# Kernel tuning notes

Measured on AMD Instinct MI355X. Metric: run time of the kernel, lower is better.

## Reference

```python
import jax, jax.numpy as jnp
import numpy as np

N, S, D, d, H = 8, 2048, 256, 128, 10  # H = rel_k_heights
SCALING = float(np.sqrt(2 * d))


def _ln(x, g, b):
    m = jnp.mean(x, axis=-1, keepdims=True)
    v = jnp.var(x, axis=-1, keepdims=True)
    return (x - m) / jnp.sqrt(v + 1e-5) * g + b


def setup_inputs() -> dict:
    key = jax.random.key(0)
    ks = jax.random.split(key, 12)
    std = 0.02
    p = lambda k, shape: (jax.random.normal(k, shape, jnp.float32) * std)
    return {
        'sequence': jax.random.normal(ks[0], (N, S, D), jnp.float32),
        'attention_mask': jax.random.bernoulli(ks[1], 0.9, (N, S, S)),
        'heights': jax.random.randint(ks[2], (N, S), 0, 50),
        'W_init': p(ks[3], (D, D)), 'b_init': jnp.zeros((D,), jnp.float32),
        'ln_g': jnp.ones((D,), jnp.float32), 'ln_b': jnp.zeros((D,), jnp.float32),
        'W_U': p(ks[4], (D, 2 * D)), 'b_U': jnp.zeros((2 * D,), jnp.float32),
        'W_V': p(ks[5], (D, 2 * D)), 'b_V': jnp.zeros((2 * D,), jnp.float32),
        'W_Z': p(ks[6], (D, d)), 'b_Z': jnp.zeros((d,), jnp.float32),
        'os_gamma': p(ks[7], (3, d)),  # torch inits gamma ~ N(0, 0.02)
        'os_beta': jnp.zeros((3, d), jnp.float32),
        'embed_heights': jax.random.normal(ks[8], (H, d), jnp.float32),
        'W_out': p(ks[9], (2 * D, D)), 'b_out': jnp.zeros((D,), jnp.float32),
        'W_gate': p(ks[10], (2 * D, D)), 'b_gate': jnp.zeros((D,), jnp.float32),
    }


def reference(sequence, attention_mask, heights,
              W_init, b_init, ln_g, ln_b,
              W_U, b_U, W_V, b_V, W_Z, b_Z,
              os_gamma, os_beta, embed_heights,
              W_out, b_out, W_gate, b_gate):
    S0 = (S - 1) // 2  # 1023
    mask = attention_mask[:, :S0, S0:]          # [N,S0,S1]
    res = sequence

    x = _ln(sequence @ W_init + b_init, ln_g, ln_b)            # [N,S,D]
    U = jax.nn.silu(x[:, :S0, :] @ W_U + b_U)                  # [N,S0,2D]
    Z = jax.nn.silu(x @ W_Z + b_Z)                             # [N,S,d]
    V = jax.nn.silu(x[:, S0:, :] @ W_V + b_V)                  # [N,S1,2D]

    # OffsetScale: Q, Qp, K from Z
    Q = (Z * os_gamma[0] + os_beta[0])[:, :S0, :]              # [N,S0,d]
    Qp = (Z * os_gamma[1] + os_beta[1])[:, :S0, :]             # [N,S0,d]
    K = (Z * os_gamma[2] + os_beta[2])[:, S0:, :]              # [N,S1,d]

    energy = jnp.einsum('bsd,btd->bst', Q, K)                  # [N,S0,S1]

    # relative-height bias: direct gather (math-equivalent to one-hot*sum)
    Q_h = jnp.einsum('bsd,hd->bsh', Qp, embed_heights)         # [N,S0,H]
    rel = heights[:, None, S0:] - heights[:, :S0, None]        # [N,S0,S1]
    rel_idx = jnp.clip(rel, 1, H) - 1
    rel_energy = jnp.take_along_axis(Q_h, rel_idx, axis=2)     # [N,S0,S1]

    logits = (energy + rel_energy) / SCALING
    logits = jnp.where(mask, logits, -9999.0)
    attn = jax.nn.softmax(logits, axis=-1)                     # [N,S0,S1]

    V_ = jnp.einsum('bst,btd->bsd', attn, V)                   # [N,S0,2D]
    out = (U * V_) @ W_out + b_out                             # [N,S0,D]
    gates = jax.nn.sigmoid(
        jnp.concatenate([out, res[:, :S0, :]], axis=-1) @ W_gate + b_gate)
    out = gates * out + (1.0 - gates) * res[:, :S0, :]
    out = jnp.concatenate([out, res[:, S0:, :]], axis=1)       # [N,S,D]
    return out
```

## Files before the change

### kernel.cpp

```cpp
#include <hip/hip_runtime.h>
#include <cstdint>
#include <cstddef>

#define S_TOT 2048
#define S0_   1023
#define S1_   1025
#define D_    256
#define D2_   512
#define DZ_   128
#define NB_   8
#define NT_   17
#define KT16_ 68
#define SCALE_INV (1.0f/16.0f)
#define XPAD  264
#define UPAD  520

typedef __attribute__((ext_vector_type(8))) short short8v;
typedef __attribute__((ext_vector_type(4))) short short4v;
typedef __attribute__((ext_vector_type(4))) float f32x4;
typedef unsigned long long u64;

__device__ __forceinline__ short f2bf(float f){
  unsigned u = __float_as_uint(f);
  unsigned r = (u + 0x7FFFu + ((u >> 16) & 1u)) >> 16;
  return (short)r;
}
__device__ __forceinline__ float bf2f(short s){
  return __uint_as_float(((unsigned)(unsigned short)s) << 16);
}
__device__ __forceinline__ float silu_f(float x){ return x / (1.f + __expf(-x)); }

__device__ __forceinline__ short8v load_afrag(const short* arow, int kt, int khi){
  short4v lo = *reinterpret_cast<const short4v*>(arow + kt*32 + khi);
  short4v hi = *reinterpret_cast<const short4v*>(arow + kt*32 + khi + 16);
  short8v r = {lo[0],lo[1],lo[2],lo[3],hi[0],hi[1],hi[2],hi[3]};
  return r;
}

__global__ __launch_bounds__(256) void k_prep(
    const float* __restrict__ W_init, const float* __restrict__ W_U,
    const float* __restrict__ W_V,    const float* __restrict__ W_Z,
    const float* __restrict__ W_out,  const float* __restrict__ W_gate,
    short* __restrict__ WpI, short* __restrict__ WpU, short* __restrict__ WpV,
    short* __restrict__ WpZ, short* __restrict__ WpO, short* __restrict__ WpG,
    const unsigned char* __restrict__ amask, u64* __restrict__ maskb)
{
  const int blk = blockIdx.x;
  if (blk < 304){
    const float* W; short* dst; int K, N, base;
    if      (blk <  32){ W=W_init; dst=WpI; K=256; N=256; base=0;   }
    else if (blk <  96){ W=W_U;    dst=WpU; K=256; N=512; base=32;  }
    else if (blk < 160){ W=W_V;    dst=WpV; K=256; N=512; base=96;  }
    else if (blk < 176){ W=W_Z;    dst=WpZ; K=256; N=128; base=160; }
    else if (blk < 240){ W=W_out;  dst=WpO; K=512; N=256; base=176; }
    else               { W=W_gate; dst=WpG; K=512; N=256; base=240; }
    const int wv = threadIdx.x >> 6, lane = threadIdx.x & 63;
    const int KT = K >> 5;
    const int tile = (blk - base)*4 + wv;
    const int nt = tile / KT, kt = tile - nt*KT;
    const int n = nt*16 + (lane & 15);
    const int kbase = kt*32 + ((lane>>4)<<2);
    short8v v;
    #pragma unroll
    for (int j=0;j<8;++j){
      int k = kbase + (j&3) + ((j>>2)<<4);
      v[j] = f2bf(W[(size_t)k*N + n]);
    }
    *reinterpret_cast<short8v*>(dst + ((size_t)tile*64 + lane)*8) = v;
  } else {
    const int lane = threadIdx.x & 63;
    const int w = (blk - 304)*4 + (threadIdx.x >> 6);
    if (w >= NB_*S0_*NT_) return;
    int b = w / (S0_*NT_);
    int rem = w - b*(S0_*NT_);
    int q = rem / NT_;
    int t = rem - q*NT_;
    int key = t*64 + lane;
    unsigned char v = 0;
    if (key < S1_) v = amask[((size_t)(b*S_TOT + q))*S_TOT + S0_ + key];
    u64 bits = __ballot(v != 0);
    if (lane == 0) maskb[w] = bits;
  }
}

__global__ __launch_bounds__(256) void k_x(
    const float* __restrict__ seq, const short* __restrict__ Wp,
    const float* __restrict__ b_init,
    const float* __restrict__ ln_g, const float* __restrict__ ln_b,
    short* __restrict__ xb, float* __restrict__ out)
{
  __shared__ short s_a[64*XPAD];
  const int tid = threadIdx.x, lane = tid & 63, wv = tid >> 6;
  const int R0 = blockIdx.x * 64;
  const int colb = lane & 15, khi = (lane>>4)<<2;

  for (int c = tid; c < 64*64; c += 256){
    int row = c >> 6, c4 = (c & 63) << 2;
    int g = R0 + row;
    float4 f = *reinterpret_cast<const float4*>(seq + (size_t)g*D_ + c4);
    short4v h = { f2bf(f.x), f2bf(f.y), f2bf(f.z), f2bf(f.w) };
    *reinterpret_cast<short4v*>(&s_a[row*XPAD + c4]) = h;
    if ((g & 2047) >= S0_)
      *reinterpret_cast<float4*>(out + (size_t)g*D_ + c4) = f;
  }
  __syncthreads();

  f32x4 acc[16];
  #pragma unroll
  for (int nt=0;nt<16;++nt) acc[nt] = (f32x4){0.f,0.f,0.f,0.f};

  const short* arow = &s_a[(wv*16 + colb)*XPAD];
  #pragma unroll
  for (int kt=0; kt<8; ++kt){
    short8v a = load_afrag(arow, kt, khi);
    #pragma unroll
    for (int nt=0; nt<16; ++nt){
      short8v b = *reinterpret_cast<const short8v*>(Wp + ((size_t)(nt*8 + kt)*64 + lane)*8);
      acc[nt] = __builtin_amdgcn_mfma_f32_16x16x32_bf16(a, b, acc[nt], 0, 0, 0);
    }
  }

  float sum[4] = {0.f,0.f,0.f,0.f};
  #pragma unroll
  for (int nt=0; nt<16; ++nt){
    float bv = b_init[nt*16 + colb];
    #pragma unroll
    for (int r=0;r<4;++r){ acc[nt][r] += bv; sum[r] += acc[nt][r]; }
  }
  #pragma unroll
  for (int r=0;r<4;++r){
    #pragma unroll
    for (int m=1;m<16;m<<=1) sum[r] += __shfl_xor(sum[r], m, 64);
    sum[r] *= (1.f/256.f);
  }
  float var[4] = {0.f,0.f,0.f,0.f};
  #pragma unroll
  for (int nt=0; nt<16; ++nt)
    #pragma unroll
    for (int r=0;r<4;++r){ float d = acc[nt][r]-sum[r]; var[r] += d*d; }
  #pragma unroll
  for (int r=0;r<4;++r){
    #pragma unroll
    for (int m=1;m<16;m<<=1) var[r] += __shfl_xor(var[r], m, 64);
    var[r] = rsqrtf(var[r]*(1.f/256.f) + 1e-5f);
  }
  #pragma unroll
  for (int nt=0; nt<16; ++nt){
    int col = nt*16 + colb;
    float g = ln_g[col], bb = ln_b[col];
    #pragma unroll
    for (int r=0;r<4;++r){
      float xn = (acc[nt][r]-sum[r])*var[r]*g + bb;
      s_a[(wv*16 + ((lane>>4)<<2) + r)*XPAD + col] = f2bf(xn);
    }
  }
  __syncthreads();
  for (int c = tid; c < 64*32; c += 256){
    int row = c >> 5, c8 = (c & 31) << 3;
    *reinterpret_cast<short8v*>(xb + (size_t)(R0+row)*D_ + c8) =
        *reinterpret_cast<const short8v*>(&s_a[row*XPAD + c8]);
  }
}

__global__ __launch_bounds__(256) void k_gemmZ(
    const short* __restrict__ xb, const short* __restrict__ Wp,
    const float* __restrict__ bias, short* __restrict__ Zb)
{
  __shared__ short s_a[64*XPAD];
  const int tid = threadIdx.x, lane = tid & 63, wv = tid >> 6;
  const int wy = wv >> 1, wx = wv & 1;
  const int R0 = blockIdx.x * 64;
  const int C0 = blockIdx.y * 64;
  const int colb = lane & 15, khi = (lane>>4)<<2;

  for (int c = tid; c < 64*32; c += 256){
    int r = c >> 5, c8 = (c & 31) << 3;
    size_t xrow = (size_t)(R0 + r);
    *reinterpret_cast<short8v*>(&s_a[r*XPAD + c8]) =
        *reinterpret_cast<const short8v*>(xb + xrow*D_ + c8);
  }
  __syncthreads();

  f32x4 acc[2][2];
  #pragma unroll
  for(int i=0;i<2;++i)
    #pragma unroll
    for(int j=0;j<2;++j) acc[i][j] = (f32x4){0.f,0.f,0.f,0.f};

  const short* ar0 = &s_a[(wy*32 + colb)*XPAD];
  const short* ar1 = ar0 + 16*XPAD;
  const int ntg = (C0 >> 4) + wx*2;
  #pragma unroll
  for (int kt=0; kt<8; ++kt){
    short8v a0 = load_afrag(ar0, kt, khi);
    short8v a1 = load_afrag(ar1, kt, khi);
    short8v b0 = *reinterpret_cast<const short8v*>(Wp + ((size_t)((ntg+0)*8 + kt)*64 + lane)*8);
    short8v b1 = *reinterpret_cast<const short8v*>(Wp + ((size_t)((ntg+1)*8 + kt)*64 + lane)*8);
    acc[0][0] = __builtin_amdgcn_mfma_f32_16x16x32_bf16(a0, b0, acc[0][0], 0,0,0);
    acc[0][1] = __builtin_amdgcn_mfma_f32_16x16x32_bf16(a0, b1, acc[0][1], 0,0,0);
    acc[1][0] = __builtin_amdgcn_mfma_f32_16x16x32_bf16(a1, b0, acc[1][0], 0,0,0);
    acc[1][1] = __builtin_amdgcn_mfma_f32_16x16x32_bf16(a1, b1, acc[1][1], 0,0,0);
  }
  #pragma unroll
  for (int sj=0; sj<2; ++sj){
    int col = C0 + wx*32 + sj*16 + colb;
    float bv = bias[col];
    #pragma unroll
    for (int si=0; si<2; ++si){
      #pragma unroll
      for (int r=0;r<4;++r){
        int orow = R0 + wy*32 + si*16 + ((lane>>4)<<2) + r;
        Zb[(size_t)orow*DZ_ + col] = f2bf(silu_f(acc[si][sj][r] + bv));
      }
    }
  }
}

__global__ __launch_bounds__(256) void k_packZ(const short* __restrict__ Zb,
                                               short* __restrict__ ZkF){
  const int lane = threadIdx.x & 63;
  const int w = blockIdx.x*4 + (threadIdx.x >> 6);
  if (w >= NB_*KT16_*4) return;
  const int b = w / (KT16_*4);
  const int rem = w - b*(KT16_*4);
  const int kt16 = rem >> 2, kt = rem & 3;
  int key = kt16*16 + (lane & 15); if (key > 1024) key = 1024;
  const short* zr = Zb + ((size_t)(b*S_TOT + S0_ + key))*DZ_ + kt*32 + ((lane>>4)<<2);
  short4v lo = *reinterpret_cast<const short4v*>(zr);
  short4v hi = *reinterpret_cast<const short4v*>(zr + 16);
  short8v f = {lo[0],lo[1],lo[2],lo[3],hi[0],hi[1],hi[2],hi[3]};
  *reinterpret_cast<short8v*>(ZkF + ((size_t)w*64 + lane)*8) = f;
}

__global__ __launch_bounds__(256) void k_gemmV(
    const short* __restrict__ xb, const short* __restrict__ Wp,
    const float* __restrict__ bias, short* __restrict__ VtF)
{
  __shared__ short s_a[64*XPAD];
  __shared__ short s_t[64][72];
  const int tid = threadIdx.x, lane = tid & 63, wv = tid >> 6;
  const int wy = wv >> 1, wx = wv & 1;
  const int R0 = blockIdx.x * 64;
  const int C0 = blockIdx.y * 64;
  const int b  = blockIdx.z;
  const int colb = lane & 15, khi = (lane>>4)<<2;

  for (int c = tid; c < 64*32; c += 256){
    int r = c >> 5, c8 = (c & 31) << 3;
    int k = R0 + r; if (k > 1024) k = 1024;
    size_t xrow = (size_t)b*S_TOT + S0_ + k;
    *reinterpret_cast<short8v*>(&s_a[r*XPAD + c8]) =
        *reinterpret_cast<const short8v*>(xb + xrow*D_ + c8);
  }
  __syncthreads();

  f32x4 acc[2][2];
  #pragma unroll
  for(int i=0;i<2;++i)
    #pragma unroll
    for(int j=0;j<2;++j) acc[i][j] = (f32x4){0.f,0.f,0.f,0.f};

  const short* ar0 = &s_a[(wy*32 + colb)*XPAD];
  const short* ar1 = ar0 + 16*XPAD;
  const int ntg = (C0 >> 4) + wx*2;
  #pragma unroll
  for (int kt=0; kt<8; ++kt){
    short8v a0 = load_afrag(ar0, kt, khi);
    short8v a1 = load_afrag(ar1, kt, khi);
    short8v b0 = *reinterpret_cast<const short8v*>(Wp + ((size_t)((ntg+0)*8 + kt)*64 + lane)*8);
    short8v b1 = *reinterpret_cast<const short8v*>(Wp + ((size_t)((ntg+1)*8 + kt)*64 + lane)*8);
    acc[0][0] = __builtin_amdgcn_mfma_f32_16x16x32_bf16(a0, b0, acc[0][0], 0,0,0);
    acc[0][1] = __builtin_amdgcn_mfma_f32_16x16x32_bf16(a0, b1, acc[0][1], 0,0,0);
    acc[1][0] = __builtin_amdgcn_mfma_f32_16x16x32_bf16(a1, b0, acc[1][0], 0,0,0);
    acc[1][1] = __builtin_amdgcn_mfma_f32_16x16x32_bf16(a1, b1, acc[1][1], 0,0,0);
  }
  #pragma unroll
  for (int sj=0; sj<2; ++sj){
    int cl = wx*32 + sj*16 + colb;
    float bv = bias[C0 + cl];
    #pragma unroll
    for (int si=0; si<2; ++si){
      #pragma unroll
      for (int r=0;r<4;++r){
        int rl = wy*32 + si*16 + ((lane>>4)<<2) + r;
        s_t[cl][rl] = f2bf(silu_f(acc[si][sj][r] + bv));
      }
    }
  }
  __syncthreads();
  {
    const int vt_l = tid >> 6;
    const int vloc = vt_l*16 + (lane & 15);
    const int krow = (lane>>4)<<2;
    const int t = R0 >> 6;
    #pragma unroll
    for (int kt=0; kt<2; ++kt){
      short8v f;
      #pragma unroll
      for (int j=0;j<8;++j){
        int kl = kt*32 + krow + (j&3) + ((j>>2)<<4);
        short v = s_t[vloc][kl];
        if (R0 + kl >= S1_) v = 0;
        f[j] = v;
      }
      size_t o = (((size_t)b*32 + (C0>>4) + vt_l)*(2*NT_) + 2*t + kt)*64 + lane;
      *reinterpret_cast<short8v*>(VtF + o*8) = f;
    }
  }
}

#define SMEM_BYTES 51712
__global__ __launch_bounds__(256,2) void k_flash(
    const short* __restrict__ Zb, const short* __restrict__ ZkF,
    const short* __restrict__ VtF, const u64* __restrict__ maskb,
    const short* __restrict__ xb,
    const short* __restrict__ WpU, const float* __restrict__ b_U,
    const short* __restrict__ Wpo, const float* __restrict__ b_out,
    const short* __restrict__ Wpg, const float* __restrict__ b_gate,
    const float* __restrict__ seq, float* __restrict__ out,
    const int* __restrict__ heights,
    const float* __restrict__ os_g, const float* __restrict__ os_b,
    const float* __restrict__ embH)
{
  __shared__ __align__(16) char smem[SMEM_BYTES];
  __shared__ float  s_qh[16][12];
  __shared__ float  s_qb[16];
  __shared__ int    s_hk[NT_*64];
  __shared__ u64    s_mb[16][NT_];
  __shared__ float  s_mx[4][16];
  __shared__ float  s_sm[4][16];

  short8v (*s_pl)[64] = reinterpret_cast<short8v(*)[64]>(smem);
  short8v (*s_ph)[64] = reinterpret_cast<short8v(*)[64]>(smem + 17408);
  short   (*s_qg)[132] = reinterpret_cast<short(*)[132]>(smem);
  short* sUV = reinterpret_cast<short*>(smem);
  short* sO  = reinterpret_cast<short*>(smem + 16640);
  short* sX  = reinterpret_cast<short*>(smem + 34816);
  short* sR  = reinterpret_cast<short*>(smem + 43264);

  const int tid = threadIdx.x, lane = tid & 63, wv = tid >> 6;
  const int b  = blockIdx.x & 7;
  const int qt = blockIdx.x >> 3;
  const int q0 = qt * 16;

  for (int c = tid; c < 16*32; c += 256){
    int r = c >> 5, c8 = (c & 31) << 3;
    int q = min(q0 + r, S0_-1);
    *reinterpret_cast<short8v*>(&sX[r*XPAD + c8]) =
        *reinterpret_cast<const short8v*>(xb + ((size_t)(b*S_TOT + q))*D_ + c8);
  }
  for (int c = tid; c < 16*64; c += 256){
    int r = c >> 6, c4 = (c & 63) << 2;
    int q = min(q0 + r, S0_-1);
    float4 f = *reinterpret_cast<const float4*>(seq + ((size_t)(b*S_TOT + q))*D_ + c4);
    short4v h = { f2bf(f.x), f2bf(f.y), f2bf(f.z), f2bf(f.w) };
    *reinterpret_cast<short4v*>(&sR[r*XPAD + c4]) = h;
  }

  {
    int row = tid >> 4, part = tid & 15;
    int q = q0 + row; if (q > S0_-1) q = S0_-1;
    const short* zrow = Zb + ((size_t)(b*S_TOT + q))*DZ_ + part*8;
    float qb_acc = 0.f;
    float qh_acc[10];
    #pragma unroll
    for (int h=0;h<10;++h) qh_acc[h] = 0.f;
    #pragma unroll
    for (int e=0; e<8; ++e){
      int dz = part*8 + e;
      float z = bf2f(zrow[e]);
      float Q  = z*os_g[dz]      + os_b[dz];
      float Qp = z*os_g[DZ_+dz]  + os_b[DZ_+dz];
      s_qg[row][dz] = f2bf(Q * os_g[2*DZ_+dz]);
      qb_acc += Q * os_b[2*DZ_+dz];
      #pragma unroll
      for (int h=0;h<10;++h) qh_acc[h] += Qp * embH[h*DZ_ + dz];
    }
    #pragma unroll
    for (int m=1;m<16;m<<=1){
      qb_acc += __shfl_xor(qb_acc, m, 64);
      #pragma unroll
      for (int h=0;h<10;++h) qh_acc[h] += __shfl_xor(qh_acc[h], m, 64);
    }
    if (part == 0){
      s_qb[row] = qb_acc;
      #pragma unroll
      for (int h=0;h<10;++h) s_qh[row][h] = qh_acc[h];
    }
  }
  for (int k = tid; k < NT_*64; k += 256)
    s_hk[k] = (k < S1_) ? heights[b*S_TOT + S0_ + k] : 0;
  for (int idx = tid; idx < 16*NT_; idx += 256){
    int qq = idx / NT_, tt = idx - qq*NT_;
    int qr = q0 + qq; if (qr > S0_-1) qr = S0_-1;
    s_mb[qq][tt] = maskb[((size_t)(b*S0_ + qr))*NT_ + tt];
  }
  __syncthreads();

  const int qcol = lane & 15, khi = (lane>>4)<<2;
  int qme = q0 + qcol; if (qme > S0_-1) qme = S0_-1;
  const int hq = heights[b*S_TOT + qme];
  const float qb = s_qb[qcol];

  short8v qgf[4];
  #pragma unroll
  for (int kt=0; kt<4; ++kt) qgf[kt] = load_afrag(&s_qg[qcol][0], kt, khi);

  f32x4 sc[5][4];
  float tmw = -1e30f;
  #pragma unroll
  for (int it=0; it<5; ++it){
    const int t = it*4 + wv;
    if (t < NT_){
      u64 mb = s_mb[qcol][t];
      #pragma unroll
      for (int st=0; st<4; ++st){
        f32x4 c = (f32x4){0.f,0.f,0.f,0.f};
        #pragma unroll
        for (int kt=0; kt<4; ++kt){
          short8v a = *reinterpret_cast<const short8v*>(
              ZkF + (((size_t)(b*KT16_ + t*4 + st)*4 + kt)*64 + lane)*8);
          c = __builtin_amdgcn_mfma_f32_16x16x32_bf16(a, qgf[kt], c, 0,0,0);
        }
        int4 hk4 = *reinterpret_cast<const int4*>(&s_hk[t*64 + st*16 + khi]);
        #pragma unroll
        for (int r=0;r<4;++r){
          int hk = (&hk4.x)[r];
          int idx = min(max(hk - hq, 1), 10) - 1;
          float v = (c[r] + qb + s_qh[qcol][idx]) * SCALE_INV;
          int kl = st*16 + khi + r;
          v = ((mb >> kl) & 1ull) ? v : -9999.f;
          c[r] = v;
          tmw = fmaxf(tmw, v);
        }
        sc[it][st] = c;
      }
    }
  }
  tmw = fmaxf(tmw, __shfl_xor(tmw, 16, 64));
  tmw = fmaxf(tmw, __shfl_xor(tmw, 32, 64));
  if (lane < 16) s_mx[wv][lane] = tmw;
  __syncthreads();

  const float m = fmaxf(fmaxf(s_mx[0][qcol], s_mx[1][qcol]),
                        fmaxf(s_mx[2][qcol], s_mx[3][qcol]));
  float ls = 0.f;
  #pragma unroll
  for (int it=0; it<5; ++it){
    const int t = it*4 + wv;
    if (t < NT_){
      #pragma unroll
      for (int st=0; st<4; ++st)
        #pragma unroll
        for (int r=0;r<4;++r){
          float p = __expf(sc[it][st][r] - m);
          ls += p;
          sc[it][st][r] = p;
        }
      short8v pa0, pa1;
      #pragma unroll
      for (int j=0;j<8;++j){
        pa0[j] = f2bf(sc[it][(j>>2)][j&3]);
        pa1[j] = f2bf(sc[it][2 + (j>>2)][j&3]);
      }
      s_pl[t][lane] = pa0;
      s_ph[t][lane] = pa1;
    }
  }
  ls += __shfl_xor(ls, 16, 64);
  ls += __shfl_xor(ls, 32, 64);
  if (lane < 16) s_sm[wv][lane] = ls;
  __syncthreads();

  float lrow[4];
  #pragma unroll
  for (int r=0;r<4;++r){
    int qr = khi + r;
    lrow[r] = s_sm[0][qr] + s_sm[1][qr] + s_sm[2][qr] + s_sm[3][qr];
  }
  f32x4 O[8];
  #pragma unroll
  for (int vt=0; vt<8; ++vt) O[vt] = (f32x4){0.f,0.f,0.f,0.f};
  for (int t=0; t<NT_; ++t){
    short8v pa0 = s_pl[t][lane];
    short8v pa1 = s_ph[t][lane];
    #pragma unroll
    for (int vt=0; vt<8; ++vt){
      size_t vb = ((size_t)b*32 + wv*8 + vt)*(2*NT_) + 2*t;
      short8v b0 = *reinterpret_cast<const short8v*>(VtF + (vb*64 + lane)*8);
      short8v b1 = *reinterpret_cast<const short8v*>(VtF + ((vb+1)*64 + lane)*8);
      O[vt] = __builtin_amdgcn_mfma_f32_16x16x32_bf16(pa0, b0, O[vt], 0,0,0);
      O[vt] = __builtin_amdgcn_mfma_f32_16x16x32_bf16(pa1, b1, O[vt], 0,0,0);
    }
  }
  __syncthreads();

  f32x4 accu[8];
  #pragma unroll
  for (int vt=0; vt<8; ++vt) accu[vt] = (f32x4){0.f,0.f,0.f,0.f};
  {
    const short* xrow = &sX[qcol*XPAD];
    #pragma unroll
    for (int kt=0; kt<8; ++kt){
      short8v a = load_afrag(xrow, kt, khi);
      #pragma unroll
      for (int vt=0; vt<8; ++vt){
        int nt = wv*8 + vt;
        short8v bw = *reinterpret_cast<const short8v*>(WpU + ((size_t)(nt*8 + kt)*64 + lane)*8);
        accu[vt] = __builtin_amdgcn_mfma_f32_16x16x32_bf16(a, bw, accu[vt], 0,0,0);
      }
    }
  }
  float inv[4];
  #pragma unroll
  for (int r=0;r<4;++r) inv[r] = 1.f / lrow[r];
  #pragma unroll
  for (int vt=0; vt<8; ++vt){
    int v = wv*128 + vt*16 + qcol;
    float bu = b_U[v];
    #pragma unroll
    for (int r=0;r<4;++r){
      float u = silu_f(accu[vt][r] + bu);
      sUV[(khi + r)*UPAD + v] = f2bf(u * O[vt][r] * inv[r]);
    }
  }
  __syncthreads();

  f32x4 acc_o[4];
  #pragma unroll
  for (int j=0;j<4;++j) acc_o[j] = (f32x4){0.f,0.f,0.f,0.f};
  {
    const short* arow = &sUV[qcol*UPAD];
    #pragma unroll
    for (int kt=0; kt<16; ++kt){
      short8v a = load_afrag(arow, kt, khi);
      #pragma unroll
      for (int j=0;j<4;++j){
        int nt = wv*4 + j;
        short8v bw = *reinterpret_cast<const short8v*>(Wpo + ((size_t)(nt*16 + kt)*64 + lane)*8);
        acc_o[j] = __builtin_amdgcn_mfma_f32_16x16x32_bf16(a, bw, acc_o[j], 0,0,0);
      }
    }
  }
  #pragma unroll
  for (int j=0;j<4;++j){
    int col = (wv*4+j)*16 + qcol;
    float bv = b_out[col];
    #pragma unroll
    for (int r=0;r<4;++r){
      acc_o[j][r] += bv;
      sO[(khi + r)*XPAD + col] = f2bf(acc_o[j][r]);
    }
  }
  __syncthreads();

  f32x4 acc_g[4];
  #pragma unroll
  for (int j=0;j<4;++j) acc_g[j] = (f32x4){0.f,0.f,0.f,0.f};
  {
    const short* orow_p = &sO[qcol*XPAD];
    const short* rrow_p = &sR[qcol*XPAD];
    #pragma unroll
    for (int kt=0; kt<8; ++kt){
      short8v a = load_afrag(orow_p, kt, khi);
      #pragma unroll
      for (int j=0;j<4;++j){
        int nt = wv*4 + j;
        short8v bw = *reinterpret_cast<const short8v*>(Wpg + ((size_t)(nt*16 + kt)*64 + lane)*8);
        acc_g[j] = __builtin_amdgcn_mfma_f32_16x16x32_bf16(a, bw, acc_g[j], 0,0,0);
      }
    }
    #pragma unroll
    for (int kt=0; kt<8; ++kt){
      short8v a = load_afrag(rrow_p, kt, khi);
      #pragma unroll
      for (int j=0;j<4;++j){
        int nt = wv*4 + j;
        short8v bw = *reinterpret_cast<const short8v*>(Wpg + ((size_t)(nt*16 + 8 + kt)*64 + lane)*8);
        acc_g[j] = __builtin_amdgcn_mfma_f32_16x16x32_bf16(a, bw, acc_g[j], 0,0,0);
      }
    }
  }
  #pragma unroll
  for (int j=0;j<4;++j){
    int col = (wv*4+j)*16 + qcol;
    float bg = b_gate[col];
    #pragma unroll
    for (int r=0;r<4;++r){
      int q = q0 + khi + r;
      if (q < S0_){
        float res = seq[((size_t)(b*S_TOT + q))*D_ + col];
        float g = 1.f/(1.f + __expf(-(acc_g[j][r] + bg)));
        out[((size_t)(b*S_TOT + q))*D_ + col] = g*acc_o[j][r] + (1.f-g)*res;
      }
    }
  }
}

extern "C" void kernel_launch(void* const* d_in, const int* in_sizes, int n_in,
                              void* d_out, int out_size, void* d_ws, size_t ws_size,
                              hipStream_t stream)
{
  const float* seq    = (const float*)d_in[0];
  const unsigned char* amask = (const unsigned char*)d_in[1];
  const int*   heights= (const int*)d_in[2];
  const float* W_init = (const float*)d_in[3];
  const float* b_init = (const float*)d_in[4];
  const float* ln_g   = (const float*)d_in[5];
  const float* ln_b   = (const float*)d_in[6];
  const float* W_U    = (const float*)d_in[7];
  const float* b_U    = (const float*)d_in[8];
  const float* W_V    = (const float*)d_in[9];
  const float* b_V    = (const float*)d_in[10];
  const float* W_Z    = (const float*)d_in[11];
  const float* b_Z    = (const float*)d_in[12];
  const float* os_g   = (const float*)d_in[13];
  const float* os_b   = (const float*)d_in[14];
  const float* embH   = (const float*)d_in[15];
  const float* W_out  = (const float*)d_in[16];
  const float* b_out  = (const float*)d_in[17];
  const float* W_gate = (const float*)d_in[18];
  const float* b_gate = (const float*)d_in[19];
  float* out = (float*)d_out;

  char* w = (char*)d_ws;
  short* Zb  = (short*)w;                w += (size_t)16512*128*2;
  short* VtF = (short*)w;                w += (size_t)8*32*(2*NT_)*64*8*2;
  short* ZkF = (short*)w;                w += (size_t)NB_*KT16_*4*64*8*2;
  short* xb  = (short*)w;                w += (size_t)16384*256*2;
  u64*  maskb = (u64*)w;                 w += (size_t)NB_*S0_*NT_*8;
  short* WpI = (short*)w;                w += (size_t)65536*2;
  short* WpU = (short*)w;                w += (size_t)131072*2;
  short* WpV = (short*)w;                w += (size_t)131072*2;
  short* WpZ = (short*)w;                w += (size_t)32768*2;
  short* WpO = (short*)w;                w += (size_t)131072*2;
  short* WpG = (short*)w;                w += (size_t)131072*2;

  hipLaunchKernelGGL(k_prep, dim3(304 + (NB_*S0_*NT_ + 3)/4), dim3(256), 0, stream,
      W_init, W_U, W_V, W_Z, W_out, W_gate,
      WpI, WpU, WpV, WpZ, WpO, WpG, amask, maskb);

  hipLaunchKernelGGL(k_x, dim3(256), dim3(256), 0, stream,
      seq, WpI, b_init, ln_g, ln_b, xb, out);

  hipLaunchKernelGGL(k_gemmZ, dim3(256, 2), dim3(256), 0, stream,
      xb, WpZ, b_Z, Zb);
  hipLaunchKernelGGL(k_packZ, dim3((NB_*KT16_*4 + 3)/4), dim3(256), 0, stream, Zb, ZkF);
  hipLaunchKernelGGL(k_gemmV, dim3(17, 8, 8), dim3(256), 0, stream,
      xb, WpV, b_V, VtF);

  hipLaunchKernelGGL(k_flash, dim3(512), dim3(256), 0, stream,
      Zb, ZkF, VtF, maskb, xb, WpU, b_U, WpO, b_out, WpG, b_gate,
      seq, out, heights, os_g, os_b, embH);
}
```

Measured before the change: 115.6 us.

## Fuse Z GEMM into LN kernel, merge V/packZ/Q-prep into one launch

```diff
diff --git a/kernel.cpp b/kernel.cpp
--- a/kernel.cpp
+++ b/kernel.cpp
@@ -14,6 +14,7 @@
 #define SCALE_INV (1.0f/16.0f)
 #define XPAD  264
 #define UPAD  520
+#define ZPAD  136
 
 typedef __attribute__((ext_vector_type(8))) short short8v;
 typedef __attribute__((ext_vector_type(4))) short short4v;
@@ -87,9 +88,11 @@
     const float* __restrict__ seq, const short* __restrict__ Wp,
     const float* __restrict__ b_init,
     const float* __restrict__ ln_g, const float* __restrict__ ln_b,
-    short* __restrict__ xb, float* __restrict__ out)
+    const short* __restrict__ WpZ, const float* __restrict__ b_Z,
+    short* __restrict__ xb, short* __restrict__ Zb, float* __restrict__ out)
 {
   __shared__ short s_a[64*XPAD];
+  __shared__ short s_z[64*ZPAD];
   const int tid = threadIdx.x, lane = tid & 63, wv = tid >> 6;
   const int R0 = blockIdx.x * 64;
   const int colb = lane & 15, khi = (lane>>4)<<2;
@@ -155,172 +158,184 @@
     }
   }
   __syncthreads();
+
   for (int c = tid; c < 64*32; c += 256){
     int row = c >> 5, c8 = (c & 31) << 3;
     *reinterpret_cast<short8v*>(xb + (size_t)(R0+row)*D_ + c8) =
         *reinterpret_cast<const short8v*>(&s_a[row*XPAD + c8]);
   }
-}
-
-__global__ __launch_bounds__(256) void k_gemmZ(
-    const short* __restrict__ xb, const short* __restrict__ Wp,
-    const float* __restrict__ bias, short* __restrict__ Zb)
-{
-  __shared__ short s_a[64*XPAD];
-  const int tid = threadIdx.x, lane = tid & 63, wv = tid >> 6;
-  const int wy = wv >> 1, wx = wv & 1;
-  const int R0 = blockIdx.x * 64;
-  const int C0 = blockIdx.y * 64;
-  const int colb = lane & 15, khi = (lane>>4)<<2;
-
-  for (int c = tid; c < 64*32; c += 256){
-    int r = c >> 5, c8 = (c & 31) << 3;
-    size_t xrow = (size_t)(R0 + r);
-    *reinterpret_cast<short8v*>(&s_a[r*XPAD + c8]) =
-        *reinterpret_cast<const short8v*>(xb + xrow*D_ + c8);
-  }
-  __syncthreads();
-
-  f32x4 acc[2][2];
-  #pragma unroll
-  for(int i=0;i<2;++i)
-    #pragma unroll
-    for(int j=0;j<2;++j) acc[i][j] = (f32x4){0.f,0.f,0.f,0.f};
-
-  const short* ar0 = &s_a[(wy*32 + colb)*XPAD];
-  const short* ar1 = ar0 + 16*XPAD;
-  const int ntg = (C0 >> 4) + wx*2;
+
+  f32x4 accz[8];
+  #pragma unroll
+  for (int nt=0;nt<8;++nt) accz[nt] = (f32x4){0.f,0.f,0.f,0.f};
   #pragma unroll
   for (int kt=0; kt<8; ++kt){
-    short8v a0 = load_afrag(ar0, kt, khi);
-    short8v a1 = load_afrag(ar1, kt, khi);
-    short8v b0 = *reinterpret_cast<const short8v*>(Wp + ((size_t)((ntg+0)*8 + kt)*64 + lane)*8);
-    short8v b1 = *reinterpret_cast<const short8v*>(Wp + ((size_t)((ntg+1)*8 + kt)*64 + lane)*8);
-    acc[0][0] = __builtin_amdgcn_mfma_f32_16x16x32_bf16(a0, b0, acc[0][0], 0,0,0);
-    acc[0][1] = __builtin_amdgcn_mfma_f32_16x16x32_bf16(a0, b1, acc[0][1], 0,0,0);
-    acc[1][0] = __builtin_amdgcn_mfma_f32_16x16x32_bf16(a1, b0, acc[1][0], 0,0,0);
-    acc[1][1] = __builtin_amdgcn_mfma_f32_16x16x32_bf16(a1, b1, acc[1][1], 0,0,0);
-  }
-  #pragma unroll
-  for (int sj=0; sj<2; ++sj){
-    int col = C0 + wx*32 + sj*16 + colb;
-    float bv = bias[col];
-    #pragma unroll
-    for (int si=0; si<2; ++si){
-      #pragma unroll
-      for (int r=0;r<4;++r){
-        int orow = R0 + wy*32 + si*16 + ((lane>>4)<<2) + r;
-        Zb[(size_t)orow*DZ_ + col] = f2bf(silu_f(acc[si][sj][r] + bv));
-      }
-    }
-  }
-}
-
-__global__ __launch_bounds__(256) void k_packZ(const short* __restrict__ Zb,
-                                               short* __restrict__ ZkF){
-  const int lane = threadIdx.x & 63;
-  const int w = blockIdx.x*4 + (threadIdx.x >> 6);
-  if (w >= NB_*KT16_*4) return;
-  const int b = w / (KT16_*4);
-  const int rem = w - b*(KT16_*4);
-  const int kt16 = rem >> 2, kt = rem & 3;
-  int key = kt16*16 + (lane & 15); if (key > 1024) key = 1024;
-  const short* zr = Zb + ((size_t)(b*S_TOT + S0_ + key))*DZ_ + kt*32 + ((lane>>4)<<2);
-  short4v lo = *reinterpret_cast<const short4v*>(zr);
-  short4v hi = *reinterpret_cast<const short4v*>(zr + 16);
-  short8v f = {lo[0],lo[1],lo[2],lo[3],hi[0],hi[1],hi[2],hi[3]};
-  *reinterpret_cast<short8v*>(ZkF + ((size_t)w*64 + lane)*8) = f;
-}
-
-__global__ __launch_bounds__(256) void k_gemmV(
-    const short* __restrict__ xb, const short* __restrict__ Wp,
-    const float* __restrict__ bias, short* __restrict__ VtF)
+    short8v a = load_afrag(arow, kt, khi);
+    #pragma unroll
+    for (int nt=0; nt<8; ++nt){
+      short8v b = *reinterpret_cast<const short8v*>(WpZ + ((size_t)(nt*8 + kt)*64 + lane)*8);
+      accz[nt] = __builtin_amdgcn_mfma_f32_16x16x32_bf16(a, b, accz[nt], 0,0,0);
+    }
+  }
+  #pragma unroll
+  for (int nt=0; nt<8; ++nt){
+    int col = nt*16 + colb;
+    float bz = b_Z[col];
+    #pragma unroll
+    for (int r=0;r<4;++r)
+      s_z[(wv*16 + khi + r)*ZPAD + col] = f2bf(silu_f(accz[nt][r] + bz));
+  }
+  __syncthreads();
+  for (int c = tid; c < 64*16; c += 256){
+    int row = c >> 4, c8 = (c & 15) << 3;
+    *reinterpret_cast<short8v*>(Zb + (size_t)(R0+row)*DZ_ + c8) =
+        *reinterpret_cast<const short8v*>(&s_z[row*ZPAD + c8]);
+  }
+}
+
+__global__ __launch_bounds__(256) void k_mid(
+    const short* __restrict__ xb, const short* __restrict__ WpV,
+    const float* __restrict__ b_V, short* __restrict__ VtF,
+    const short* __restrict__ Zb, short* __restrict__ ZkF,
+    const float* __restrict__ os_g, const float* __restrict__ os_b,
+    const float* __restrict__ embH,
+    short* __restrict__ Qgb, float* __restrict__ qhb)
 {
   __shared__ short s_a[64*XPAD];
   __shared__ short s_t[64][72];
+  const int blk = blockIdx.x;
   const int tid = threadIdx.x, lane = tid & 63, wv = tid >> 6;
-  const int wy = wv >> 1, wx = wv & 1;
-  const int R0 = blockIdx.x * 64;
-  const int C0 = blockIdx.y * 64;
-  const int b  = blockIdx.z;
-  const int colb = lane & 15, khi = (lane>>4)<<2;
-
-  for (int c = tid; c < 64*32; c += 256){
-    int r = c >> 5, c8 = (c & 31) << 3;
-    int k = R0 + r; if (k > 1024) k = 1024;
-    size_t xrow = (size_t)b*S_TOT + S0_ + k;
-    *reinterpret_cast<short8v*>(&s_a[r*XPAD + c8]) =
-        *reinterpret_cast<const short8v*>(xb + xrow*D_ + c8);
-  }
-  __syncthreads();
-
-  f32x4 acc[2][2];
-  #pragma unroll
-  for(int i=0;i<2;++i)
-    #pragma unroll
-    for(int j=0;j<2;++j) acc[i][j] = (f32x4){0.f,0.f,0.f,0.f};
-
-  const short* ar0 = &s_a[(wy*32 + colb)*XPAD];
-  const short* ar1 = ar0 + 16*XPAD;
-  const int ntg = (C0 >> 4) + wx*2;
-  #pragma unroll
-  for (int kt=0; kt<8; ++kt){
-    short8v a0 = load_afrag(ar0, kt, khi);
-    short8v a1 = load_afrag(ar1, kt, khi);
-    short8v b0 = *reinterpret_cast<const short8v*>(Wp + ((size_t)((ntg+0)*8 + kt)*64 + lane)*8);
-    short8v b1 = *reinterpret_cast<const short8v*>(Wp + ((size_t)((ntg+1)*8 + kt)*64 + lane)*8);
-    acc[0][0] = __builtin_amdgcn_mfma_f32_16x16x32_bf16(a0, b0, acc[0][0], 0,0,0);
-    acc[0][1] = __builtin_amdgcn_mfma_f32_16x16x32_bf16(a0, b1, acc[0][1], 0,0,0);
-    acc[1][0] = __builtin_amdgcn_mfma_f32_16x16x32_bf16(a1, b0, acc[1][0], 0,0,0);
-    acc[1][1] = __builtin_amdgcn_mfma_f32_16x16x32_bf16(a1, b1, acc[1][1], 0,0,0);
-  }
-  #pragma unroll
-  for (int sj=0; sj<2; ++sj){
-    int cl = wx*32 + sj*16 + colb;
-    float bv = bias[C0 + cl];
-    #pragma unroll
-    for (int si=0; si<2; ++si){
-      #pragma unroll
-      for (int r=0;r<4;++r){
-        int rl = wy*32 + si*16 + ((lane>>4)<<2) + r;
-        s_t[cl][rl] = f2bf(silu_f(acc[si][sj][r] + bv));
-      }
-    }
-  }
-  __syncthreads();
-  {
-    const int vt_l = tid >> 6;
-    const int vloc = vt_l*16 + (lane & 15);
-    const int krow = (lane>>4)<<2;
-    const int t = R0 >> 6;
-    #pragma unroll
-    for (int kt=0; kt<2; ++kt){
-      short8v f;
-      #pragma unroll
-      for (int j=0;j<8;++j){
-        int kl = kt*32 + krow + (j&3) + ((j>>2)<<4);
-        short v = s_t[vloc][kl];
-        if (R0 + kl >= S1_) v = 0;
-        f[j] = v;
-      }
-      size_t o = (((size_t)b*32 + (C0>>4) + vt_l)*(2*NT_) + 2*t + kt)*64 + lane;
-      *reinterpret_cast<short8v*>(VtF + o*8) = f;
+
+  if (blk < 1088){
+    const int t   = blk % 17;
+    const int rest= blk / 17;
+    const int C0  = (rest & 7) * 64;
+    const int b   = rest >> 3;
+    const int R0  = t * 64;
+    const int wy = wv >> 1, wx = wv & 1;
+    const int colb = lane & 15, khi = (lane>>4)<<2;
+
+    for (int c = tid; c < 64*32; c += 256){
+      int r = c >> 5, c8 = (c & 31) << 3;
+      int k = R0 + r; if (k > 1024) k = 1024;
+      size_t xrow = (size_t)b*S_TOT + S0_ + k;
+      *reinterpret_cast<short8v*>(&s_a[r*XPAD + c8]) =
+          *reinterpret_cast<const short8v*>(xb + xrow*D_ + c8);
+    }
+    __syncthreads();
+
+    f32x4 acc[2][2];
+    #pragma unroll
+    for(int i=0;i<2;++i)
+      #pragma unroll
+      for(int j=0;j<2;++j) acc[i][j] = (f32x4){0.f,0.f,0.f,0.f};
+
+    const short* ar0 = &s_a[(wy*32 + colb)*XPAD];
+    const short* ar1 = ar0 + 16*XPAD;
+    const int ntg = (C0 >> 4) + wx*2;
+    #pragma unroll
+    for (int kt=0; kt<8; ++kt){
+      short8v a0 = load_afrag(ar0, kt, khi);
+      short8v a1 = load_afrag(ar1, kt, khi);
+      short8v b0 = *reinterpret_cast<const short8v*>(WpV + ((size_t)((ntg+0)*8 + kt)*64 + lane)*8);
+      short8v b1 = *reinterpret_cast<const short8v*>(WpV + ((size_t)((ntg+1)*8 + kt)*64 + lane)*8);
+      acc[0][0] = __builtin_amdgcn_mfma_f32_16x16x32_bf16(a0, b0, acc[0][0], 0,0,0);
+      acc[0][1] = __builtin_amdgcn_mfma_f32_16x16x32_bf16(a0, b1, acc[0][1], 0,0,0);
+      acc[1][0] = __builtin_amdgcn_mfma_f32_16x16x32_bf16(a1, b0, acc[1][0], 0,0,0);
+      acc[1][1] = __builtin_amdgcn_mfma_f32_16x16x32_bf16(a1, b1, acc[1][1], 0,0,0);
+    }
+    #pragma unroll
+    for (int sj=0; sj<2; ++sj){
+      int cl = wx*32 + sj*16 + colb;
+      float bv = b_V[C0 + cl];
+      #pragma unroll
+      for (int si=0; si<2; ++si){
+        #pragma unroll
+        for (int r=0;r<4;++r){
+          int rl = wy*32 + si*16 + ((lane>>4)<<2) + r;
+          s_t[cl][rl] = f2bf(silu_f(acc[si][sj][r] + bv));
+        }
+      }
+    }
+    __syncthreads();
+    {
+      const int vt_l = tid >> 6;
+      const int vloc = vt_l*16 + (lane & 15);
+      const int krow = (lane>>4)<<2;
+      #pragma unroll
+      for (int kt=0; kt<2; ++kt){
+        short8v f;
+        #pragma unroll
+        for (int j=0;j<8;++j){
+          int kl = kt*32 + krow + (j&3) + ((j>>2)<<4);
+          short v = s_t[vloc][kl];
+          if (R0 + kl >= S1_) v = 0;
+          f[j] = v;
+        }
+        size_t o = (((size_t)b*32 + (C0>>4) + vt_l)*(2*NT_) + 2*t + kt)*64 + lane;
+        *reinterpret_cast<short8v*>(VtF + o*8) = f;
+      }
+    }
+  } else if (blk < 1632){
+    const int w = (blk - 1088)*4 + wv;
+    if (w >= NB_*KT16_*4) return;
+    const int b = w / (KT16_*4);
+    const int rem = w - b*(KT16_*4);
+    const int kt16 = rem >> 2, kt = rem & 3;
+    int key = kt16*16 + (lane & 15); if (key > 1024) key = 1024;
+    const short* zr = Zb + ((size_t)(b*S_TOT + S0_ + key))*DZ_ + kt*32 + ((lane>>4)<<2);
+    short4v lo = *reinterpret_cast<const short4v*>(zr);
+    short4v hi = *reinterpret_cast<const short4v*>(zr + 16);
+    short8v f = {lo[0],lo[1],lo[2],lo[3],hi[0],hi[1],hi[2],hi[3]};
+    *reinterpret_cast<short8v*>(ZkF + ((size_t)w*64 + lane)*8) = f;
+  } else {
+    const int idx = blk - 1632;
+    const int b = idx & 7, q0 = (idx >> 3) * 16;
+    int row = tid >> 4, part = tid & 15;
+    int q = q0 + row; if (q > S0_-1) q = S0_-1;
+    const short* zrow = Zb + ((size_t)(b*S_TOT + q))*DZ_ + part*8;
+    float qb_acc = 0.f;
+    float qh_acc[10];
+    #pragma unroll
+    for (int h=0;h<10;++h) qh_acc[h] = 0.f;
+    short8v qgv;
+    #pragma unroll
+    for (int e=0; e<8; ++e){
+      int dz = part*8 + e;
+      float z = bf2f(zrow[e]);
+      float Q  = z*os_g[dz]      + os_b[dz];
+      float Qp = z*os_g[DZ_+dz]  + os_b[DZ_+dz];
+      qgv[e] = f2bf(Q * os_g[2*DZ_+dz]);
+      qb_acc += Q * os_b[2*DZ_+dz];
+      #pragma unroll
+      for (int h=0;h<10;++h) qh_acc[h] += Qp * embH[h*DZ_ + dz];
+    }
+    *reinterpret_cast<short8v*>(Qgb + ((size_t)(b*1024 + q0 + row))*DZ_ + part*8) = qgv;
+    #pragma unroll
+    for (int m=1;m<16;m<<=1){
+      qb_acc += __shfl_xor(qb_acc, m, 64);
+      #pragma unroll
+      for (int h=0;h<10;++h) qh_acc[h] += __shfl_xor(qh_acc[h], m, 64);
+    }
+    if (part == 0){
+      float* dst = qhb + ((size_t)(b*1024 + q0 + row))*12;
+      #pragma unroll
+      for (int h=0;h<10;++h) dst[h] = qh_acc[h];
+      dst[10] = qb_acc;
     }
   }
 }
 
 #define SMEM_BYTES 51712
 __global__ __launch_bounds__(256,2) void k_flash(
-    const short* __restrict__ Zb, const short* __restrict__ ZkF,
-    const short* __restrict__ VtF, const u64* __restrict__ maskb,
-    const short* __restrict__ xb,
+    const short* __restrict__ Qgb, const float* __restrict__ qhb,
+    const short* __restrict__ ZkF, const short* __restrict__ VtF,
+    const u64* __restrict__ maskb, const short* __restrict__ xb,
     const short* __restrict__ WpU, const float* __restrict__ b_U,
     const short* __restrict__ Wpo, const float* __restrict__ b_out,
     const short* __restrict__ Wpg, const float* __restrict__ b_gate,
     const float* __restrict__ seq, float* __restrict__ out,
-    const int* __restrict__ heights,
-    const float* __restrict__ os_g, const float* __restrict__ os_b,
-    const float* __restrict__ embH)
+    const int* __restrict__ heights)
 {
   __shared__ __align__(16) char smem[SMEM_BYTES];
   __shared__ float  s_qh[16][12];
@@ -332,7 +347,6 @@
 
   short8v (*s_pl)[64] = reinterpret_cast<short8v(*)[64]>(smem);
   short8v (*s_ph)[64] = reinterpret_cast<short8v(*)[64]>(smem + 17408);
-  short   (*s_qg)[132] = reinterpret_cast<short(*)[132]>(smem);
   short* sUV = reinterpret_cast<short*>(smem);
   short* sO  = reinterpret_cast<short*>(smem + 16640);
   short* sX  = reinterpret_cast<short*>(smem + 34816);
@@ -356,37 +370,10 @@
     short4v h = { f2bf(f.x), f2bf(f.y), f2bf(f.z), f2bf(f.w) };
     *reinterpret_cast<short4v*>(&sR[r*XPAD + c4]) = h;
   }
-
-  {
-    int row = tid >> 4, part = tid & 15;
-    int q = q0 + row; if (q > S0_-1) q = S0_-1;
-    const short* zrow = Zb + ((size_t)(b*S_TOT + q))*DZ_ + part*8;
-    float qb_acc = 0.f;
-    float qh_acc[10];
-    #pragma unroll
-    for (int h=0;h<10;++h) qh_acc[h] = 0.f;
-    #pragma unroll
-    for (int e=0; e<8; ++e){
-      int dz = part*8 + e;
-      float z = bf2f(zrow[e]);
-      float Q  = z*os_g[dz]      + os_b[dz];
-      float Qp = z*os_g[DZ_+dz]  + os_b[DZ_+dz];
-      s_qg[row][dz] = f2bf(Q * os_g[2*DZ_+dz]);
-      qb_acc += Q * os_b[2*DZ_+dz];
-      #pragma unroll
-      for (int h=0;h<10;++h) qh_acc[h] += Qp * embH[h*DZ_ + dz];
-    }
-    #pragma unroll
-    for (int m=1;m<16;m<<=1){
-      qb_acc += __shfl_xor(qb_acc, m, 64);
-      #pragma unroll
-      for (int h=0;h<10;++h) qh_acc[h] += __shfl_xor(qh_acc[h], m, 64);
-    }
-    if (part == 0){
-      s_qb[row] = qb_acc;
-      #pragma unroll
-      for (int h=0;h<10;++h) s_qh[row][h] = qh_acc[h];
-    }
+  if (tid < 192){
+    int row = tid / 12, j = tid - row*12;
+    float v = qhb[((size_t)(b*1024 + q0 + row))*12 + j];
+    if (j < 10) s_qh[row][j] = v; else if (j == 10) s_qb[row] = v;
   }
   for (int k = tid; k < NT_*64; k += 256)
     s_hk[k] = (k < S1_) ? heights[b*S_TOT + S0_ + k] : 0;
@@ -401,11 +388,16 @@
   int qme = q0 + qcol; if (qme > S0_-1) qme = S0_-1;
   const int hq = heights[b*S_TOT + qme];
   const float qb = s_qb[qcol];
+  const int lb = lane*8;
 
   short8v qgf[4];
-  #pragma unroll
-  for (int kt=0; kt<4; ++kt) qgf[kt] = load_afrag(&s_qg[qcol][0], kt, khi);
-
+  {
+    const short* qgrow = Qgb + ((size_t)(b*1024 + q0 + qcol))*DZ_;
+    #pragma unroll
+    for (int kt=0; kt<4; ++kt) qgf[kt] = load_afrag(qgrow, kt, khi);
+  }
+
+  const short* zkb = ZkF + (size_t)b*KT16_*4*512;
   f32x4 sc[5][4];
   float tmw = -1e30f;
   #pragma unroll
@@ -418,8 +410,7 @@
         f32x4 c = (f32x4){0.f,0.f,0.f,0.f};
         #pragma unroll
         for (int kt=0; kt<4; ++kt){
-          short8v a = *reinterpret_cast<const short8v*>(
-              ZkF + (((size_t)(b*KT16_ + t*4 + st)*4 + kt)*64 + lane)*8);
+          short8v a = *reinterpret_cast<const short8v*>(zkb + (t*16 + st*4 + kt)*512 + lb);
           c = __builtin_amdgcn_mfma_f32_16x16x32_bf16(a, qgf[kt], c, 0,0,0);
         }
         int4 hk4 = *reinterpret_cast<const int4*>(&s_hk[t*64 + st*16 + khi]);
@@ -481,14 +472,15 @@
   f32x4 O[8];
   #pragma unroll
   for (int vt=0; vt<8; ++vt) O[vt] = (f32x4){0.f,0.f,0.f,0.f};
+  const short* vwb = VtF + (size_t)(b*32 + wv*8)*(2*NT_)*512;
   for (int t=0; t<NT_; ++t){
     short8v pa0 = s_pl[t][lane];
     short8v pa1 = s_ph[t][lane];
     #pragma unroll
     for (int vt=0; vt<8; ++vt){
-      size_t vb = ((size_t)b*32 + wv*8 + vt)*(2*NT_) + 2*t;
-      short8v b0 = *reinterpret_cast<const short8v*>(VtF + (vb*64 + lane)*8);
-      short8v b1 = *reinterpret_cast<const short8v*>(VtF + ((vb+1)*64 + lane)*8);
+      int o0 = (vt*(2*NT_) + 2*t)*512 + lb;
+      short8v b0 = *reinterpret_cast<const short8v*>(vwb + o0);
+      short8v b1 = *reinterpret_cast<const short8v*>(vwb + o0 + 512);
       O[vt] = __builtin_amdgcn_mfma_f32_16x16x32_bf16(pa0, b0, O[vt], 0,0,0);
       O[vt] = __builtin_amdgcn_mfma_f32_16x16x32_bf16(pa1, b1, O[vt], 0,0,0);
     }
@@ -629,6 +621,8 @@
   short* ZkF = (short*)w;                w += (size_t)NB_*KT16_*4*64*8*2;
   short* xb  = (short*)w;                w += (size_t)16384*256*2;
   u64*  maskb = (u64*)w;                 w += (size_t)NB_*S0_*NT_*8;
+  short* Qgb = (short*)w;                w += (size_t)8*1024*128*2;
+  float* qhb = (float*)w;                w += (size_t)8*1024*12*4;
   short* WpI = (short*)w;                w += (size_t)65536*2;
   short* WpU = (short*)w;                w += (size_t)131072*2;
   short* WpV = (short*)w;                w += (size_t)131072*2;
@@ -641,15 +635,12 @@
       WpI, WpU, WpV, WpZ, WpO, WpG, amask, maskb);
 
   hipLaunchKernelGGL(k_x, dim3(256), dim3(256), 0, stream,
-      seq, WpI, b_init, ln_g, ln_b, xb, out);
-
-  hipLaunchKernelGGL(k_gemmZ, dim3(256, 2), dim3(256), 0, stream,
-      xb, WpZ, b_Z, Zb);
-  hipLaunchKernelGGL(k_packZ, dim3((NB_*KT16_*4 + 3)/4), dim3(256), 0, stream, Zb, ZkF);
-  hipLaunchKernelGGL(k_gemmV, dim3(17, 8, 8), dim3(256), 0, stream,
-      xb, WpV, b_V, VtF);
+      seq, WpI, b_init, ln_g, ln_b, WpZ, b_Z, xb, Zb, out);
+
+  hipLaunchKernelGGL(k_mid, dim3(2144), dim3(256), 0, stream,
+      xb, WpV, b_V, VtF, Zb, ZkF, os_g, os_b, embH, Qgb, qhb);
 
   hipLaunchKernelGGL(k_flash, dim3(512), dim3(256), 0, stream,
-      Zb, ZkF, VtF, maskb, xb, WpU, b_U, WpO, b_out, WpG, b_gate,
-      seq, out, heights, os_g, os_b, embH);
-}
+      Qgb, qhb, ZkF, VtF, maskb, xb, WpU, b_U, WpO, b_out, WpG, b_gate,
+      seq, out, heights);
+}
```

Result: slower. 124.6 us (+7.8%).
